# Performance work log

Measured on AMD Instinct MI355X. Metric: run time of the kernel, lower is better.

Reference implementation:

```python
import jax, jax.numpy as jnp
import numpy as np

N_T, N_C, N_M = 300000, 100000, 20000
D_IN, D, D_OUT = 390, 128, 64
H_PRE, H_POST = 256, 64


def _nrm(k, shape, scale=0.02):
    return jax.random.normal(k, shape, dtype=jnp.float32) * scale


def setup_inputs() -> dict:
    key = jax.random.key(0)
    ks = jax.random.split(key, 24)
    inp = {
        'input_features': jax.random.normal(ks[0], (N_T, D_IN), jnp.float32),
        'card_of_target': jax.random.randint(ks[1], (N_T,), 0, N_C, jnp.int32),
        'merchant_of_target': jax.random.randint(ks[2], (N_T,), 0, N_M, jnp.int32),
        # HeteroEmbedding tables for src types feeding 'target'
        'card_emb': _nrm(ks[3], (N_C, D)),
        'merch_emb': _nrm(ks[4], (N_M, D)),
        # target_preprocessing FFBlock (390 -> 256 -> 128, n_layers=2)
        'pre_Wi': _nrm(ks[5], (D_IN, H_PRE)), 'pre_bi': jnp.zeros((H_PRE,), jnp.float32),
        'pre_Wh': _nrm(ks[6], (H_PRE, H_PRE)), 'pre_bh': jnp.zeros((H_PRE,), jnp.float32),
        'pre_Wo': _nrm(ks[7], (H_PRE, D)), 'pre_bo': jnp.zeros((D,), jnp.float32),
        # conv1 / conv2: one GraphConv per etype; order:
        # 0=card->target, 1=merchant->target, 2=target->card, 3=target->merchant
        'conv1_W': _nrm(ks[8], (4, D, D)), 'conv1_b': jnp.zeros((4, D), jnp.float32),
        'conv2_W': _nrm(ks[9], (4, D, D)), 'conv2_b': jnp.zeros((4, D), jnp.float32),
        # conv3: dst=='target' -> D_OUT; dst!='target' -> 1
        'conv3_Wt': _nrm(ks[10], (2, D, D_OUT)), 'conv3_bt': jnp.zeros((2, D_OUT), jnp.float32),
        'conv3_Wo': _nrm(ks[11], (2, D, 1)), 'conv3_bo': jnp.zeros((2, 1), jnp.float32),
        # target_postprocessing FFBlock (64 -> 64 -> 1, n_layers=2)
        'post_Wi': _nrm(ks[12], (D_OUT, H_POST)), 'post_bi': jnp.zeros((H_POST,), jnp.float32),
        'post_Wh': _nrm(ks[13], (H_POST, H_POST)), 'post_bh': jnp.zeros((H_POST,), jnp.float32),
        'post_Wo': _nrm(ks[14], (H_POST, 1)), 'post_bo': jnp.zeros((1,), jnp.float32),
    }
    return inp


def _ff(x, Wi, bi, Wh, bh, Wo, bo, n_layers=2):
    h = jax.nn.relu(x @ Wi + bi)
    for _ in range(1, n_layers):
        h = jax.nn.relu(h @ Wh + bh)
    return h @ Wo + bo


def _deg(ids, n):
    # degree per node over edge endpoint list, clamped to >= 1 (DGL GraphConv)
    return jnp.maximum(jnp.zeros((n,), jnp.float32).at[ids].add(1.0), 1.0)


def _gconv(x_src, src, dst, n_dst, W, b, d_src, d_dst):
    # DGL GraphConv, norm='both': scale src by out_deg^-1/2, matmul,
    # sum messages onto dst, scale by in_deg^-1/2, add bias.
    h = (x_src * jax.lax.rsqrt(d_src)[:, None]) @ W          # [n_src, out]
    agg = jax.ops.segment_sum(h[src], dst, num_segments=n_dst)
    return agg * jax.lax.rsqrt(d_dst)[:, None] + b


def reference(input_features, card_of_target, merchant_of_target,
              card_emb, merch_emb,
              pre_Wi, pre_bi, pre_Wh, pre_bh, pre_Wo, pre_bo,
              conv1_W, conv1_b, conv2_W, conv2_b,
              conv3_Wt, conv3_bt, conv3_Wo, conv3_bo,
              post_Wi, post_bi, post_Wh, post_bh, post_Wo, post_bo):
    n_t, n_c, n_m = input_features.shape[0], card_emb.shape[0], merch_emb.shape[0]
    t_ids = jnp.arange(n_t, dtype=jnp.int32)
    d_c = _deg(card_of_target, n_c)      # card degree (in/out symmetric here)
    d_m = _deg(merchant_of_target, n_m)  # merchant degree
    d_t = _deg(t_ids, n_t)               # target degree (=1 per etype)

    tf = _ff(input_features, pre_Wi, pre_bi, pre_Wh, pre_bh, pre_Wo, pre_bo)

    # conv1 (HeteroGraphConv, aggregate='sum') + relu
    h1_t = (_gconv(card_emb, card_of_target, t_ids, n_t, conv1_W[0], conv1_b[0], d_c, d_t)
            + _gconv(merch_emb, merchant_of_target, t_ids, n_t, conv1_W[1], conv1_b[1], d_m, d_t))
    h1_c = _gconv(tf, t_ids, card_of_target, n_c, conv1_W[2], conv1_b[2], d_t, d_c)
    h1_m = _gconv(tf, t_ids, merchant_of_target, n_m, conv1_W[3], conv1_b[3], d_t, d_m)
    h1_t, h1_c, h1_m = jax.nn.relu(h1_t), jax.nn.relu(h1_c), jax.nn.relu(h1_m)

    # conv2 applied (conv_layers - 2) = 1 time
    h2_t, h2_c, h2_m = h1_t, h1_c, h1_m
    for _ in range(2, 3):
        n_t2 = (_gconv(h2_c, card_of_target, t_ids, n_t, conv2_W[0], conv2_b[0], d_c, d_t)
                + _gconv(h2_m, merchant_of_target, t_ids, n_t, conv2_W[1], conv2_b[1], d_m, d_t))
        n_c2 = _gconv(h2_t, t_ids, card_of_target, n_c, conv2_W[2], conv2_b[2], d_t, d_c)
        n_m2 = _gconv(h2_t, t_ids, merchant_of_target, n_m, conv2_W[3], conv2_b[3], d_t, d_m)
        h2_t, h2_c, h2_m = jax.nn.relu(n_t2), jax.nn.relu(n_c2), jax.nn.relu(n_m2)

    # conv3: D_OUT into target, 1 into non-target dsts; no relu
    h3_t = (_gconv(h2_c, card_of_target, t_ids, n_t, conv3_Wt[0], conv3_bt[0], d_c, d_t)
            + _gconv(h2_m, merchant_of_target, t_ids, n_t, conv3_Wt[1], conv3_bt[1], d_m, d_t))
    h3_c = _gconv(h2_t, t_ids, card_of_target, n_c, conv3_Wo[0], conv3_bo[0], d_t, d_c)
    h3_m = _gconv(h2_t, t_ids, merchant_of_target, n_m, conv3_Wo[1], conv3_bo[1], d_t, d_m)

    h3_t = _ff(h3_t, post_Wi, post_bi, post_Wh, post_bh, post_Wo, post_bo)
    return h3_t, h3_c, h3_m
```

## Files before the change

### kernel.cpp

```cpp
#include <hip/hip_runtime.h>


#define NT 300000
#define NC 100000
#define NM 20000
#define DIN 390
#define DD 128
#define DOUT 64
#define HPRE 256
#define HPOST 64

typedef _Float16 half8 __attribute__((ext_vector_type(8)));
typedef float f32x16 __attribute__((ext_vector_type(16)));
typedef float f32x4 __attribute__((ext_vector_type(4)));

#define LO_SCALE 512.0f
#define LO_INV   (1.0f / 512.0f)

__device__ __forceinline__ void split2(float x, _Float16& h, _Float16& l) {
    _Float16 hh = (_Float16)x;
    h = hh;
    l = (_Float16)((x - (float)hh) * LO_SCALE);
}

template<int TM, int TN, int WGM, int WGN>
__global__ __launch_bounds__(256, 3) void gemm_mfma(
    const float* __restrict__ A, const _Float16* __restrict__ Wh,
    const _Float16* __restrict__ Wl, const float* __restrict__ bias,
    const float* __restrict__ rowscale, float* __restrict__ C,
    int M, int K, int N, int Kpad, int relu)
{
    constexpr int BM = 32 * TM * WGM;
    constexpr int BN = 32 * TN * WGN;
    constexpr int RS = 40;
    __shared__ __align__(16) _Float16 Ah[BM * RS];
    __shared__ __align__(16) _Float16 Al[BM * RS];
    __shared__ __align__(16) _Float16 Bh[BN * RS];
    __shared__ __align__(16) _Float16 Bl[BN * RS];

    const int tid  = (int)threadIdx.x;
    const int lane = tid & 63;
    const int wave = tid >> 6;
    const int wm0 = (wave % WGM) * 32 * TM;
    const int wn0 = (wave / WGM) * 32 * TN;

    const int nbn = N / BN;
    const int tile = (int)blockIdx.x;
    const int bm = (tile / nbn) * BM;
    const int bn = (tile % nbn) * BN;

    f32x16 zz;
    #pragma unroll
    for (int i = 0; i < 16; ++i) zz[i] = 0.f;
    f32x16 acc_hh[TM][TN], acc_x[TM][TN];
    #pragma unroll
    for (int tm = 0; tm < TM; ++tm)
        #pragma unroll
        for (int tn = 0; tn < TN; ++tn) { acc_hh[tm][tn] = zz; acc_x[tm][tn] = zz; }

    constexpr int TPR  = 256 / BM;
    constexpr int KPT  = 32 / TPR;
    constexpr int FQ   = KPT / 4;
    const int sar = tid / TPR;
    const int sak = (tid % TPR) * KPT;
    const int agrow = bm + sar;
    const float* Aptr = A + (size_t)agrow * K;

    constexpr int TPRB = 256 / BN;
    constexpr int KPTB = 32 / TPRB;
    constexpr int NB   = KPTB / 8;
    const int sbr = tid / TPRB;
    const int sbk = (tid % TPRB) * KPTB;
    const _Float16* Bhp = Wh + (size_t)(bn + sbr) * Kpad + sbk;
    const _Float16* Blp = Wl + (size_t)(bn + sbr) * Kpad + sbk;

    const int ml  = lane & 31;
    const int klo = (lane >> 5) * 8;

    f32x4 areg[FQ];
    half8 bhreg[NB], blreg[NB];

    auto loadA = [&](int k0) {
        #pragma unroll
        for (int q = 0; q < FQ; ++q) {
            const int kb = k0 + sak + q * 4;
            f32x4 f = {0.f, 0.f, 0.f, 0.f};
            if (agrow < M) {
                if (kb + 3 < K) {
                    f = *(const f32x4*)(Aptr + kb);
                } else {
                    if (kb + 0 < K) f[0] = Aptr[kb + 0];
                    if (kb + 1 < K) f[1] = Aptr[kb + 1];
                    if (kb + 2 < K) f[2] = Aptr[kb + 2];
                    if (kb + 3 < K) f[3] = Aptr[kb + 3];
                }
            }
            areg[q] = f;
        }
    };
    auto loadB = [&](int k0) {
        #pragma unroll
        for (int j = 0; j < NB; ++j) {
            bhreg[j] = *(const half8*)(Bhp + k0 + j * 8);
            blreg[j] = *(const half8*)(Blp + k0 + j * 8);
        }
    };

    loadA(0);
    loadB(0);

    for (int k0 = 0; k0 < K; k0 += 32) {
        #pragma unroll
        for (int c = 0; c < FQ / 2; ++c) {
            half8 h, l;
            #pragma unroll
            for (int q = 0; q < 2; ++q) {
                #pragma unroll
                for (int j = 0; j < 4; ++j) {
                    _Float16 th, tl;
                    split2(areg[2 * c + q][j], th, tl);
                    h[q * 4 + j] = th;
                    l[q * 4 + j] = tl;
                }
            }
            *(half8*)&Ah[sar * RS + sak + c * 8] = h;
            *(half8*)&Al[sar * RS + sak + c * 8] = l;
        }
        #pragma unroll
        for (int j = 0; j < NB; ++j) {
            *(half8*)&Bh[sbr * RS + sbk + j * 8] = bhreg[j];
            *(half8*)&Bl[sbr * RS + sbk + j * 8] = blreg[j];
        }
        __syncthreads();

        if (k0 + 32 < K) { loadA(k0 + 32); loadB(k0 + 32); }

        #pragma unroll
        for (int ks = 0; ks < 2; ++ks) {
            const int kk = ks * 16 + klo;
            half8 fah[TM], fal[TM], fbh[TN], fbl[TN];
            #pragma unroll
            for (int t = 0; t < TM; ++t) {
                const int m = wm0 + t * 32 + ml;
                fah[t] = *(const half8*)&Ah[m * RS + kk];
                fal[t] = *(const half8*)&Al[m * RS + kk];
            }
            #pragma unroll
            for (int t = 0; t < TN; ++t) {
                const int n = wn0 + t * 32 + ml;
                fbh[t] = *(const half8*)&Bh[n * RS + kk];
                fbl[t] = *(const half8*)&Bl[n * RS + kk];
            }
            #pragma unroll
            for (int tm = 0; tm < TM; ++tm)
                #pragma unroll
                for (int tn = 0; tn < TN; ++tn) {
                    acc_hh[tm][tn] = __builtin_amdgcn_mfma_f32_32x32x16_f16(
                        fah[tm], fbh[tn], acc_hh[tm][tn], 0, 0, 0);
                    acc_x[tm][tn] = __builtin_amdgcn_mfma_f32_32x32x16_f16(
                        fah[tm], fbl[tn], acc_x[tm][tn], 0, 0, 0);
                    acc_x[tm][tn] = __builtin_amdgcn_mfma_f32_32x32x16_f16(
                        fal[tm], fbh[tn], acc_x[tm][tn], 0, 0, 0);
                }
        }
        __syncthreads();
    }

    const int r0 = 4 * (lane >> 5);
    #pragma unroll
    for (int tm = 0; tm < TM; ++tm) {
        #pragma unroll
        for (int tn = 0; tn < TN; ++tn) {
            const int gcol = bn + wn0 + tn * 32 + ml;
            const float bc = (bias != nullptr) ? bias[gcol] : 0.f;
            #pragma unroll
            for (int r = 0; r < 16; ++r) {
                const int grow = bm + wm0 + tm * 32 + (r & 3) + r0 + 8 * (r >> 2);
                if (grow < M) {
                    float v = acc_hh[tm][tn][r] + acc_x[tm][tn][r] * LO_INV;
                    if (rowscale != nullptr) v *= rowscale[grow];
                    v += bc;
                    if (relu) v = fmaxf(v, 0.f);
                    C[(size_t)grow * N + gcol] = v;
                }
            }
        }
    }
}

__global__ void split_w(const float* __restrict__ W, _Float16* __restrict__ hiT,
                        _Float16* __restrict__ loT, int K, int N, int Kpad, int nmat)
{
    int idx = blockIdx.x * blockDim.x + threadIdx.x;
    int total = nmat * N * Kpad;
    if (idx >= total) return;
    int e = idx / (N * Kpad);
    int rem = idx - e * (N * Kpad);
    int n = rem / Kpad;
    int k = rem - n * Kpad;
    float v = (k < K) ? W[((size_t)e * K + k) * N + n] : 0.f;
    _Float16 h = (_Float16)v;
    hiT[idx] = h;
    loT[idx] = (_Float16)((v - (float)h) * LO_SCALE);
}

__global__ void count_kernel(const int* __restrict__ card, const int* __restrict__ merch,
                             int* cnt_c, int* cnt_m, int n)
{
    int t = blockIdx.x * blockDim.x + threadIdx.x;
    if (t >= n) return;
    atomicAdd(&cnt_c[card[t]], 1);
    atomicAdd(&cnt_m[merch[t]], 1);
}

__global__ void rsqrt_kernel(const int* __restrict__ cnt, float* __restrict__ rs, int n)
{
    int i = blockIdx.x * blockDim.x + threadIdx.x;
    if (i >= n) return;
    int c = cnt[i];
    if (c < 1) c = 1;
    rs[i] = 1.0f / sqrtf((float)c);
}

__global__ __launch_bounds__(1024) void scan_excl(const int* __restrict__ cnt,
                                                  int* __restrict__ off, int n)
{
    __shared__ int wsum[16];
    const int tid = (int)threadIdx.x;
    const int lane = tid & 63, wid = tid >> 6;
    int carry = 0;
    for (int base = 0; base < n; base += 1024) {
        int i = base + tid;
        int v = (i < n) ? cnt[i] : 0;
        int x = v;
        #pragma unroll
        for (int d = 1; d < 64; d <<= 1) {
            int y = __shfl_up(x, d);
            if (lane >= d) x += y;
        }
        if (lane == 63) wsum[wid] = x;
        __syncthreads();
        int wpre = 0, tot = 0;
        #pragma unroll
        for (int w = 0; w < 16; ++w) {
            int s = wsum[w];
            if (w < wid) wpre += s;
            tot += s;
        }
        if (i < n) off[i] = carry + wpre + (x - v);
        carry += tot;
        __syncthreads();
    }
    if (tid == 0) off[n] = carry;
}

__global__ void fill_sorted(const int* __restrict__ ids, const int* __restrict__ off,
                            int* cur, int* __restrict__ srt, int n)
{
    int t = blockIdx.x * blockDim.x + threadIdx.x;
    if (t >= n) return;
    int c = ids[t];
    int p = atomicAdd(&cur[c], 1);
    srt[off[c] + p] = t;
}

__global__ void gather2_kernel(const float* __restrict__ hc, const float* __restrict__ hm,
                               const int* __restrict__ card, const int* __restrict__ merch,
                               const float* __restrict__ b0, const float* __restrict__ b1,
                               float* __restrict__ out, int n, int dim, int relu)
{
    int idx = blockIdx.x * blockDim.x + threadIdx.x;
    int per = dim >> 2;
    int t = idx / per;
    if (t >= n) return;
    int d4 = (idx % per) << 2;
    int c = card[t], m = merch[t];
    float4 a = *(const float4*)(hc + (size_t)c * dim + d4);
    float4 b = *(const float4*)(hm + (size_t)m * dim + d4);
    float4 v0 = *(const float4*)(b0 + d4);
    float4 v1 = *(const float4*)(b1 + d4);
    float4 r;
    r.x = a.x + b.x + v0.x + v1.x;
    r.y = a.y + b.y + v0.y + v1.y;
    r.z = a.z + b.z + v0.z + v1.z;
    r.w = a.w + b.w + v0.w + v1.w;
    if (relu) {
        r.x = fmaxf(r.x, 0.f); r.y = fmaxf(r.y, 0.f);
        r.z = fmaxf(r.z, 0.f); r.w = fmaxf(r.w, 0.f);
    }
    *(float4*)(out + (size_t)t * dim + d4) = r;
}

__global__ __launch_bounds__(256) void agg_csr_kernel(
    const float* __restrict__ proj, const int* __restrict__ off,
    const int* __restrict__ srt, const float* __restrict__ rs,
    const float* __restrict__ bias, float* __restrict__ out, int n, int relu)
{
    int node = blockIdx.x * 2 + ((int)threadIdx.x >> 7);
    int d = (int)threadIdx.x & 127;
    if (node >= n) return;
    int s = off[node], e = off[node + 1];
    float acc = 0.f;
    for (int i = s; i < e; ++i) {
        int t = srt[i];
        acc += proj[(size_t)t * 128 + d];
    }
    float v = acc * rs[node] + bias[d];
    if (relu) v = fmaxf(v, 0.f);
    out[(size_t)node * 128 + d] = v;
}

__global__ __launch_bounds__(256) void dot2_kernel(
    const float* __restrict__ h, const float* __restrict__ w0,
    const float* __restrict__ w1, float* __restrict__ s2, int n)
{
    int row = blockIdx.x * 4 + ((int)threadIdx.x >> 6);
    int l = (int)threadIdx.x & 63;
    if (row >= n) return;
    const float* x = h + (size_t)row * 128;
    float x0 = x[l], x1 = x[l + 64];
    float p0 = x0 * w0[l] + x1 * w0[l + 64];
    float p1 = x0 * w1[l] + x1 * w1[l + 64];
    #pragma unroll
    for (int o = 32; o > 0; o >>= 1) {
        p0 += __shfl_down(p0, o);
        p1 += __shfl_down(p1, o);
    }
    if (l == 0) { s2[(size_t)row * 2] = p0; s2[(size_t)row * 2 + 1] = p1; }
}

__global__ void agg_scalar_kernel(const float* __restrict__ s2, int which,
                                  const int* __restrict__ off, const int* __restrict__ srt,
                                  const float* __restrict__ rs, const float* __restrict__ bias,
                                  float* __restrict__ out, int n)
{
    int node = blockIdx.x * blockDim.x + threadIdx.x;
    if (node >= n) return;
    float acc = 0.f;
    int e = off[node + 1];
    for (int i = off[node]; i < e; ++i) acc += s2[(size_t)srt[i] * 2 + which];
    out[node] = acc * rs[node] + bias[0];
}

__global__ __launch_bounds__(256) void dot1_kernel(
    const float* __restrict__ h, const float* __restrict__ w,
    const float* __restrict__ b, float* __restrict__ out, int n)
{
    int row = blockIdx.x * 4 + ((int)threadIdx.x >> 6);
    int l = (int)threadIdx.x & 63;
    if (row >= n) return;
    float p = h[(size_t)row * 64 + l] * w[l];
    #pragma unroll
    for (int o = 32; o > 0; o >>= 1) p += __shfl_down(p, o);
    if (l == 0) out[row] = p + b[0];
}

static inline void gemmN(const float* A, const _Float16* wh, const _Float16* wl,
                         const float* bias, const float* rs, float* C,
                         int M, int K, int N, int Kpad, int relu, hipStream_t s)
{
    const int nbm = (M + 63) / 64;
    if (N % 128 == 0) {
        const int nbn = N / 128;
        gemm_mfma<1, 2, 2, 2><<<dim3(nbm * nbn), 256, 0, s>>>(
            A, wh, wl, bias, rs, C, M, K, N, Kpad, relu);
    } else {
        gemm_mfma<1, 1, 2, 2><<<dim3(nbm), 256, 0, s>>>(
            A, wh, wl, bias, rs, C, M, K, N, Kpad, relu);
    }
}

extern "C" void kernel_launch(void* const* d_in, const int* in_sizes, int n_in,
                              void* d_out, int out_size, void* d_ws, size_t ws_size,
                              hipStream_t stream)
{
    const float* x_in      = (const float*)d_in[0];
    const int*   card      = (const int*)d_in[1];
    const int*   merch     = (const int*)d_in[2];
    const float* card_emb  = (const float*)d_in[3];
    const float* merch_emb = (const float*)d_in[4];
    const float* pre_Wi = (const float*)d_in[5];
    const float* pre_bi = (const float*)d_in[6];
    const float* pre_Wh = (const float*)d_in[7];
    const float* pre_bh = (const float*)d_in[8];
    const float* pre_Wo = (const float*)d_in[9];
    const float* pre_bo = (const float*)d_in[10];
    const float* conv1_W = (const float*)d_in[11];
    const float* conv1_b = (const float*)d_in[12];
    const float* conv2_W = (const float*)d_in[13];
    const float* conv2_b = (const float*)d_in[14];
    const float* conv3_Wt = (const float*)d_in[15];
    const float* conv3_bt = (const float*)d_in[16];
    const float* conv3_Wo = (const float*)d_in[17];
    const float* conv3_bo = (const float*)d_in[18];
    const float* post_Wi = (const float*)d_in[19];
    const float* post_bi = (const float*)d_in[20];
    const float* post_Wh = (const float*)d_in[21];
    const float* post_bh = (const float*)d_in[22];
    const float* post_Wo = (const float*)d_in[23];
    const float* post_bo = (const float*)d_in[24];

    float* out = (float*)d_out;

    char* ws = (char*)d_ws;
    size_t off = 0;
    auto alloc = [&](size_t bytes) -> char* {
        char* p = ws + off;
        off += (bytes + 255) & ~(size_t)255;
        return p;
    };
    int* cnt_c = (int*)alloc((size_t)NC * 4);
    int* cnt_m = (int*)alloc((size_t)NM * 4);
    int* cur_c = (int*)alloc((size_t)NC * 4);
    int* cur_m = (int*)alloc((size_t)NM * 4);
    size_t zero_bytes = (size_t)((char*)(cur_m + NM) - (char*)cnt_c);
    int* off_c = (int*)alloc((size_t)(NC + 1) * 4);
    int* off_m = (int*)alloc((size_t)(NM + 1) * 4);
    int* srt_c = (int*)alloc((size_t)NT * 4);
    int* srt_m = (int*)alloc((size_t)NT * 4);
    float* rs_c = (float*)alloc((size_t)NC * 4);
    float* rs_m = (float*)alloc((size_t)NM * 4);

    const int KP_WI = 416;
    _Float16* wi_h  = (_Float16*)alloc((size_t)HPRE * KP_WI * 2);
    _Float16* wi_l  = (_Float16*)alloc((size_t)HPRE * KP_WI * 2);
    _Float16* wh_h  = (_Float16*)alloc((size_t)HPRE * HPRE * 2);
    _Float16* wh_l  = (_Float16*)alloc((size_t)HPRE * HPRE * 2);
    _Float16* wo_h  = (_Float16*)alloc((size_t)DD * HPRE * 2);
    _Float16* wo_l  = (_Float16*)alloc((size_t)DD * HPRE * 2);
    _Float16* c1_h  = (_Float16*)alloc((size_t)4 * DD * DD * 2);
    _Float16* c1_l  = (_Float16*)alloc((size_t)4 * DD * DD * 2);
    _Float16* c2_h  = (_Float16*)alloc((size_t)4 * DD * DD * 2);
    _Float16* c2_l  = (_Float16*)alloc((size_t)4 * DD * DD * 2);
    _Float16* c3_h  = (_Float16*)alloc((size_t)2 * DOUT * DD * 2);
    _Float16* c3_l  = (_Float16*)alloc((size_t)2 * DOUT * DD * 2);
    _Float16* pi_h  = (_Float16*)alloc((size_t)HPOST * DOUT * 2);
    _Float16* pi_l  = (_Float16*)alloc((size_t)HPOST * DOUT * 2);
    _Float16* ph_h  = (_Float16*)alloc((size_t)HPOST * HPOST * 2);
    _Float16* ph_l  = (_Float16*)alloc((size_t)HPOST * HPOST * 2);

    float* bufA = (float*)alloc((size_t)NT * HPRE * 4);
    float* bufB = (float*)alloc((size_t)NT * HPRE * 4);
    float* tf   = (float*)alloc((size_t)NT * DD * 4);
    float* proj = (float*)alloc((size_t)NT * DD * 4);
    float* h1_t = (float*)alloc((size_t)NT * DD * 4);
    float* h2_t = (float*)alloc((size_t)NT * DD * 4);
    float* h1_c = (float*)alloc((size_t)NC * DD * 4);
    float* h2_c = (float*)alloc((size_t)NC * DD * 4);
    float* hc_p = (float*)alloc((size_t)NC * DD * 4);
    float* h1_m = (float*)alloc((size_t)NM * DD * 4);
    float* h2_m = (float*)alloc((size_t)NM * DD * 4);
    float* hm_p = (float*)alloc((size_t)NM * DD * 4);
    float* s2   = (float*)alloc((size_t)NT * 2 * 4);
    float* h3t64 = h1_t;
    float* p1 = h2_t;
    float* p2 = h2_t + (size_t)NT * 64;
    (void)ws_size; (void)in_sizes; (void)n_in; (void)out_size;

    hipMemsetAsync(cnt_c, 0, zero_bytes, stream);
    count_kernel<<<(NT + 255) / 256, 256, 0, stream>>>(card, merch, cnt_c, cnt_m, NT);
    rsqrt_kernel<<<(NC + 255) / 256, 256, 0, stream>>>(cnt_c, rs_c, NC);
    rsqrt_kernel<<<(NM + 255) / 256, 256, 0, stream>>>(cnt_m, rs_m, NM);
    scan_excl<<<1, 1024, 0, stream>>>(cnt_c, off_c, NC);
    scan_excl<<<1, 1024, 0, stream>>>(cnt_m, off_m, NM);
    fill_sorted<<<(NT + 255) / 256, 256, 0, stream>>>(card, off_c, cur_c, srt_c, NT);
    fill_sorted<<<(NT + 255) / 256, 256, 0, stream>>>(merch, off_m, cur_m, srt_m, NT);

    auto splitw = [&](const float* W, _Float16* h, _Float16* l, int K, int N, int Kpad, int nmat) {
        int total = nmat * N * Kpad;
        split_w<<<(total + 255) / 256, 256, 0, stream>>>(W, h, l, K, N, Kpad, nmat);
    };
    splitw(pre_Wi,   wi_h, wi_l, DIN,  HPRE,  KP_WI, 1);
    splitw(pre_Wh,   wh_h, wh_l, HPRE, HPRE,  HPRE,  1);
    splitw(pre_Wo,   wo_h, wo_l, HPRE, DD,    HPRE,  1);
    splitw(conv1_W,  c1_h, c1_l, DD,   DD,    DD,    4);
    splitw(conv2_W,  c2_h, c2_l, DD,   DD,    DD,    4);
    splitw(conv3_Wt, c3_h, c3_l, DD,   DOUT,  DD,    2);
    splitw(post_Wi,  pi_h, pi_l, DOUT, HPOST, DOUT,  1);
    splitw(post_Wh,  ph_h, ph_l, HPOST,HPOST, HPOST, 1);

    const int WP = DD * DD;

    gemmN(x_in, wi_h, wi_l, pre_bi, nullptr, bufA, NT, DIN,  HPRE, KP_WI, 1, stream);
    gemmN(bufA, wh_h, wh_l, pre_bh, nullptr, bufB, NT, HPRE, HPRE, HPRE,  1, stream);
    gemmN(bufB, wo_h, wo_l, pre_bo, nullptr, tf,   NT, HPRE, DD,   HPRE,  0, stream);

    gemmN(card_emb,  c1_h + 0 * WP, c1_l + 0 * WP, nullptr, rs_c, hc_p, NC, DD, DD, DD, 0, stream);
    gemmN(merch_emb, c1_h + 1 * WP, c1_l + 1 * WP, nullptr, rs_m, hm_p, NM, DD, DD, DD, 0, stream);
    gather2_kernel<<<(NT * (DD / 4) + 255) / 256, 256, 0, stream>>>(
        hc_p, hm_p, card, merch, conv1_b, conv1_b + DD, h1_t, NT, DD, 1);
    gemmN(tf, c1_h + 2 * WP, c1_l + 2 * WP, nullptr, nullptr, proj, NT, DD, DD, DD, 0, stream);
    agg_csr_kernel<<<(NC + 1) / 2, 256, 0, stream>>>(proj, off_c, srt_c, rs_c,
                                                     conv1_b + 2 * DD, h1_c, NC, 1);
    gemmN(tf, c1_h + 3 * WP, c1_l + 3 * WP, nullptr, nullptr, proj, NT, DD, DD, DD, 0, stream);
    agg_csr_kernel<<<(NM + 1) / 2, 256, 0, stream>>>(proj, off_m, srt_m, rs_m,
                                                     conv1_b + 3 * DD, h1_m, NM, 1);

    gemmN(h1_c, c2_h + 0 * WP, c2_l + 0 * WP, nullptr, rs_c, hc_p, NC, DD, DD, DD, 0, stream);
    gemmN(h1_m, c2_h + 1 * WP, c2_l + 1 * WP, nullptr, rs_m, hm_p, NM, DD, DD, DD, 0, stream);
    gather2_kernel<<<(NT * (DD / 4) + 255) / 256, 256, 0, stream>>>(
        hc_p, hm_p, card, merch, conv2_b, conv2_b + DD, h2_t, NT, DD, 1);
    gemmN(h1_t, c2_h + 2 * WP, c2_l + 2 * WP, nullptr, nullptr, proj, NT, DD, DD, DD, 0, stream);
    agg_csr_kernel<<<(NC + 1) / 2, 256, 0, stream>>>(proj, off_c, srt_c, rs_c,
                                                     conv2_b + 2 * DD, h2_c, NC, 1);
    gemmN(h1_t, c2_h + 3 * WP, c2_l + 3 * WP, nullptr, nullptr, proj, NT, DD, DD, DD, 0, stream);
    agg_csr_kernel<<<(NM + 1) / 2, 256, 0, stream>>>(proj, off_m, srt_m, rs_m,
                                                     conv2_b + 3 * DD, h2_m, NM, 1);

    const int WP3 = DOUT * DD;
    gemmN(h2_c, c3_h + 0 * WP3, c3_l + 0 * WP3, nullptr, rs_c, hc_p, NC, DD, DOUT, DD, 0, stream);
    gemmN(h2_m, c3_h + 1 * WP3, c3_l + 1 * WP3, nullptr, rs_m, hm_p, NM, DD, DOUT, DD, 0, stream);
    gather2_kernel<<<(NT * (DOUT / 4) + 255) / 256, 256, 0, stream>>>(
        hc_p, hm_p, card, merch, conv3_bt, conv3_bt + DOUT, h3t64, NT, DOUT, 0);
    dot2_kernel<<<(NT + 3) / 4, 256, 0, stream>>>(h2_t, conv3_Wo, conv3_Wo + DD, s2, NT);
    agg_scalar_kernel<<<(NC + 255) / 256, 256, 0, stream>>>(s2, 0, off_c, srt_c, rs_c,
                                                            conv3_bo + 0, out + NT, NC);
    agg_scalar_kernel<<<(NM + 255) / 256, 256, 0, stream>>>(s2, 1, off_m, srt_m, rs_m,
                                                            conv3_bo + 1, out + NT + NC, NM);

    gemmN(h3t64, pi_h, pi_l, post_bi, nullptr, p1, NT, DOUT,  HPOST, DOUT,  1, stream);
    gemmN(p1,    ph_h, ph_l, post_bh, nullptr, p2, NT, HPOST, HPOST, HPOST, 1, stream);
    dot1_kernel<<<(NT + 3) / 4, 256, 0, stream>>>(p2, post_Wo, post_bo, out, NT);
}
```

Measured before the change: 2.791 ms.

## Store activations as pre-split fp16 hi/lo pairs and add direct-to-LDS GEMM

Producers (GEMM epilogues, gather, CSR aggregation) now write activations as fp16 hi/lo pairs instead of fp32. A new 512-thread GEMM loads these pre-split operands straight into LDS with global_load_lds, double-buffered and XOR-swizzled. This removes the per-tile fp32-to-fp16 split inside the GEMM and keeps total activation traffic the same (two fp16 halves equal one fp32), while the extra split kernels for the embedding tables add some one-off work. Buffers are padded to multiples of 128 rows so the loads need no bounds checks.

```diff
diff --git a/kernel.cpp b/kernel.cpp
--- a/kernel.cpp
+++ b/kernel.cpp
@@ -11,6 +11,7 @@
 #define HPOST 64
 
 typedef _Float16 half8 __attribute__((ext_vector_type(8)));
+typedef _Float16 half4v __attribute__((ext_vector_type(4)));
 typedef float f32x16 __attribute__((ext_vector_type(16)));
 typedef float f32x4 __attribute__((ext_vector_type(4)));
 
@@ -23,11 +24,147 @@
     l = (_Float16)((x - (float)hh) * LO_SCALE);
 }
 
+__device__ __forceinline__ void gload16(const _Float16* g, _Float16* l) {
+    __builtin_amdgcn_global_load_lds(
+        (const __attribute__((address_space(1))) void*)g,
+        (__attribute__((address_space(3))) void*)l, 16, 0, 0);
+}
+
+template<int TN>
+__global__ __launch_bounds__(512, 4) void gemm_ps(
+    const _Float16* __restrict__ Agh, const _Float16* __restrict__ Agl,
+    const _Float16* __restrict__ Bgh, const _Float16* __restrict__ Bgl,
+    const float* __restrict__ bias, const float* __restrict__ rowscale,
+    _Float16* __restrict__ Ch, _Float16* __restrict__ Cl,
+    float* __restrict__ C32,
+    int M, int Kpad, int N, int relu)
+{
+    constexpr int BM = 128;
+    constexpr int BN = 64 * TN;
+    constexpr int OFF_AH = 0;
+    constexpr int OFF_AL = 4096;
+    constexpr int OFF_BH = 8192;
+    constexpr int OFF_BL = 8192 + BN * 32;
+    constexpr int BUFH   = 8192 + 2 * BN * 32;
+    constexpr int NLD    = (TN == 2) ? 4 : 3;
+    __shared__ __align__(16) _Float16 smem[2 * BUFH];
+
+    const int tid  = (int)threadIdx.x;
+    const int lane = tid & 63;
+    const int wave = tid >> 6;
+    const int wm0  = (wave & 3) * 32;
+    const int wn0  = (wave >> 2) * 32 * TN;
+
+    const int nbn  = N / BN;
+    const int bm   = ((int)blockIdx.x / nbn) * BM;
+    const int bn   = ((int)blockIdx.x % nbn) * BN;
+
+    const int srow = lane >> 2;
+    const int xc8  = (((lane & 3) ^ (srow & 3)) << 3);
+    const size_t a_off = (size_t)(bm + wave * 16 + srow) * Kpad + xc8;
+    size_t b_off;
+    if constexpr (TN == 2) {
+        b_off = (size_t)(bn + wave * 16 + srow) * Kpad + xc8;
+    } else {
+        b_off = (size_t)(bn + (wave & 3) * 16 + srow) * Kpad + xc8;
+    }
+
+    auto stage = [&](int b, int k0) {
+        _Float16* sb = &smem[b * BUFH];
+        gload16(Agh + a_off + k0, sb + OFF_AH + wave * 512);
+        gload16(Agl + a_off + k0, sb + OFF_AL + wave * 512);
+        if constexpr (TN == 2) {
+            gload16(Bgh + b_off + k0, sb + OFF_BH + wave * 512);
+            gload16(Bgl + b_off + k0, sb + OFF_BL + wave * 512);
+        } else {
+            gload16((wave < 4 ? Bgh : Bgl) + b_off + k0,
+                    sb + (wave < 4 ? OFF_BH : OFF_BL) + (wave & 3) * 512);
+        }
+    };
+
+    f32x16 zz;
+    #pragma unroll
+    for (int i = 0; i < 16; ++i) zz[i] = 0.f;
+    f32x16 acc_hh[TN], acc_x[TN];
+    #pragma unroll
+    for (int t2 = 0; t2 < TN; ++t2) { acc_hh[t2] = zz; acc_x[t2] = zz; }
+
+    const int mlr = lane & 31;
+    const int hi5 = lane >> 5;
+    const int xr  = mlr & 3;
+
+    const int NS = Kpad >> 5;
+    stage(0, 0);
+
+    for (int t = 0; t < NS; ++t) {
+        if (t + 1 < NS) {
+            stage((t + 1) & 1, (t + 1) << 5);
+            asm volatile("s_waitcnt vmcnt(%0)" :: "n"(NLD) : "memory");
+        } else {
+            asm volatile("s_waitcnt vmcnt(0)" ::: "memory");
+        }
+        __builtin_amdgcn_s_barrier();
+        __builtin_amdgcn_sched_barrier(0);
+
+        const _Float16* sb = &smem[(t & 1) * BUFH];
+        #pragma unroll
+        for (int ks = 0; ks < 2; ++ks) {
+            const int xo = (((ks * 2 + hi5) ^ xr) << 3);
+            const half8 fah = *(const half8*)&sb[OFF_AH + (wm0 + mlr) * 32 + xo];
+            const half8 fal = *(const half8*)&sb[OFF_AL + (wm0 + mlr) * 32 + xo];
+            half8 fbh[TN], fbl[TN];
+            #pragma unroll
+            for (int t2 = 0; t2 < TN; ++t2) {
+                const int nn = wn0 + t2 * 32 + mlr;
+                fbh[t2] = *(const half8*)&sb[OFF_BH + nn * 32 + xo];
+                fbl[t2] = *(const half8*)&sb[OFF_BL + nn * 32 + xo];
+            }
+            #pragma unroll
+            for (int t2 = 0; t2 < TN; ++t2) {
+                acc_hh[t2] = __builtin_amdgcn_mfma_f32_32x32x16_f16(
+                    fah, fbh[t2], acc_hh[t2], 0, 0, 0);
+                acc_x[t2] = __builtin_amdgcn_mfma_f32_32x32x16_f16(
+                    fah, fbl[t2], acc_x[t2], 0, 0, 0);
+                acc_x[t2] = __builtin_amdgcn_mfma_f32_32x32x16_f16(
+                    fal, fbh[t2], acc_x[t2], 0, 0, 0);
+            }
+        }
+        __builtin_amdgcn_sched_barrier(0);
+        __builtin_amdgcn_s_barrier();
+    }
+
+    const int r0 = 4 * hi5;
+    #pragma unroll
+    for (int t2 = 0; t2 < TN; ++t2) {
+        const int gcol = bn + wn0 + t2 * 32 + mlr;
+        const float bc = (bias != nullptr) ? bias[gcol] : 0.f;
+        #pragma unroll
+        for (int r = 0; r < 16; ++r) {
+            const int grow = bm + wm0 + (r & 3) + r0 + 8 * (r >> 2);
+            if (grow < M) {
+                float v = acc_hh[t2][r] + acc_x[t2][r] * LO_INV;
+                if (rowscale != nullptr) v *= rowscale[grow];
+                v += bc;
+                if (relu) v = fmaxf(v, 0.f);
+                if (C32 != nullptr) {
+                    C32[(size_t)grow * N + gcol] = v;
+                } else {
+                    _Float16 hh, ll;
+                    split2(v, hh, ll);
+                    Ch[(size_t)grow * N + gcol] = hh;
+                    Cl[(size_t)grow * N + gcol] = ll;
+                }
+            }
+        }
+    }
+}
+
 template<int TM, int TN, int WGM, int WGN>
 __global__ __launch_bounds__(256, 3) void gemm_mfma(
     const float* __restrict__ A, const _Float16* __restrict__ Wh,
     const _Float16* __restrict__ Wl, const float* __restrict__ bias,
-    const float* __restrict__ rowscale, float* __restrict__ C,
+    const float* __restrict__ rowscale,
+    float* __restrict__ C32, _Float16* __restrict__ Ch, _Float16* __restrict__ Cl,
     int M, int K, int N, int Kpad, int relu)
 {
     constexpr int BM = 32 * TM * WGM;
@@ -181,7 +318,14 @@
                     if (rowscale != nullptr) v *= rowscale[grow];
                     v += bc;
                     if (relu) v = fmaxf(v, 0.f);
-                    C[(size_t)grow * N + gcol] = v;
+                    if (C32 != nullptr) {
+                        C32[(size_t)grow * N + gcol] = v;
+                    } else {
+                        _Float16 hh, ll;
+                        split2(v, hh, ll);
+                        Ch[(size_t)grow * N + gcol] = hh;
+                        Cl[(size_t)grow * N + gcol] = ll;
+                    }
                 }
             }
         }
@@ -204,6 +348,31 @@
     loT[idx] = (_Float16)((v - (float)h) * LO_SCALE);
 }
 
+__global__ void split_a(const float* __restrict__ X, _Float16* __restrict__ xh,
+                        _Float16* __restrict__ xl, int M, int Mpad, int K)
+{
+    int idx = blockIdx.x * blockDim.x + threadIdx.x;
+    int per = K >> 3;
+    int total = Mpad * per;
+    if (idx >= total) return;
+    int row = idx / per;
+    int k = (idx - row * per) << 3;
+    half8 h, l;
+    if (row < M) {
+        #pragma unroll
+        for (int j = 0; j < 8; ++j) {
+            _Float16 th, tl;
+            split2(X[(size_t)row * K + k + j], th, tl);
+            h[j] = th; l[j] = tl;
+        }
+    } else {
+        #pragma unroll
+        for (int j = 0; j < 8; ++j) { h[j] = (_Float16)0.f; l[j] = (_Float16)0.f; }
+    }
+    *(half8*)&xh[(size_t)row * K + k] = h;
+    *(half8*)&xl[(size_t)row * K + k] = l;
+}
+
 __global__ void count_kernel(const int* __restrict__ card, const int* __restrict__ merch,
                              int* cnt_c, int* cnt_m, int n)
 {
@@ -267,7 +436,8 @@
 __global__ void gather2_kernel(const float* __restrict__ hc, const float* __restrict__ hm,
                                const int* __restrict__ card, const int* __restrict__ merch,
                                const float* __restrict__ b0, const float* __restrict__ b1,
-                               float* __restrict__ out, int n, int dim, int relu)
+                               float* __restrict__ out32, _Float16* __restrict__ oh,
+                               _Float16* __restrict__ ol, int n, int dim, int relu)
 {
     int idx = blockIdx.x * blockDim.x + threadIdx.x;
     int per = dim >> 2;
@@ -288,13 +458,25 @@
         r.x = fmaxf(r.x, 0.f); r.y = fmaxf(r.y, 0.f);
         r.z = fmaxf(r.z, 0.f); r.w = fmaxf(r.w, 0.f);
     }
-    *(float4*)(out + (size_t)t * dim + d4) = r;
+    if (out32 != nullptr) {
+        *(float4*)(out32 + (size_t)t * dim + d4) = r;
+    } else {
+        half4v h, l;
+        _Float16 th, tl;
+        split2(r.x, th, tl); h[0] = th; l[0] = tl;
+        split2(r.y, th, tl); h[1] = th; l[1] = tl;
+        split2(r.z, th, tl); h[2] = th; l[2] = tl;
+        split2(r.w, th, tl); h[3] = th; l[3] = tl;
+        *(half4v*)&oh[(size_t)t * dim + d4] = h;
+        *(half4v*)&ol[(size_t)t * dim + d4] = l;
+    }
 }
 
 __global__ __launch_bounds__(256) void agg_csr_kernel(
     const float* __restrict__ proj, const int* __restrict__ off,
     const int* __restrict__ srt, const float* __restrict__ rs,
-    const float* __restrict__ bias, float* __restrict__ out, int n, int relu)
+    const float* __restrict__ bias, _Float16* __restrict__ oh,
+    _Float16* __restrict__ ol, int n, int relu)
 {
     int node = blockIdx.x * 2 + ((int)threadIdx.x >> 7);
     int d = (int)threadIdx.x & 127;
@@ -307,7 +489,10 @@
     }
     float v = acc * rs[node] + bias[d];
     if (relu) v = fmaxf(v, 0.f);
-    out[(size_t)node * 128 + d] = v;
+    _Float16 hh, ll;
+    split2(v, hh, ll);
+    oh[(size_t)node * 128 + d] = hh;
+    ol[(size_t)node * 128 + d] = ll;
 }
 
 __global__ __launch_bounds__(256) void dot2_kernel(
@@ -355,20 +540,22 @@
     if (l == 0) out[row] = p + b[0];
 }
 
-static inline void gemmN(const float* A, const _Float16* wh, const _Float16* wl,
-                         const float* bias, const float* rs, float* C,
-                         int M, int K, int N, int Kpad, int relu, hipStream_t s)
-{
-    const int nbm = (M + 63) / 64;
+static inline void gemm_ps_launch(const _Float16* Ah, const _Float16* Al,
+    const _Float16* Bh, const _Float16* Bl, const float* bias, const float* rs,
+    _Float16* Ch, _Float16* Cl, float* C32,
+    int M, int Kpad, int N, int relu, hipStream_t s)
+{
+    const int nbm = (M + 127) / 128;
     if (N % 128 == 0) {
-        const int nbn = N / 128;
-        gemm_mfma<1, 2, 2, 2><<<dim3(nbm * nbn), 256, 0, s>>>(
-            A, wh, wl, bias, rs, C, M, K, N, Kpad, relu);
+        gemm_ps<2><<<dim3(nbm * (N / 128)), 512, 0, s>>>(
+            Ah, Al, Bh, Bl, bias, rs, Ch, Cl, C32, M, Kpad, N, relu);
     } else {
-        gemm_mfma<1, 1, 2, 2><<<dim3(nbm), 256, 0, s>>>(
-            A, wh, wl, bias, rs, C, M, K, N, Kpad, relu);
-    }
-}
+        gemm_ps<1><<<dim3(nbm), 512, 0, s>>>(
+            Ah, Al, Bh, Bl, bias, rs, Ch, Cl, C32, M, Kpad, N, relu);
+    }
+}
+
+#define PAD128(x) ((((x) + 127) / 128) * 128)
 
 extern "C" void kernel_launch(void* const* d_in, const int* in_sizes, int n_in,
                               void* d_out, int out_size, void* d_ws, size_t ws_size,
@@ -402,6 +589,10 @@
 
     float* out = (float*)d_out;
 
+    const int MTP = PAD128(NT);
+    const int MCP = PAD128(NC);
+    const int MMP = PAD128(NM);
+
     char* ws = (char*)d_ws;
     size_t off = 0;
     auto alloc = [&](size_t bytes) -> char* {
@@ -439,22 +630,37 @@
     _Float16* ph_h  = (_Float16*)alloc((size_t)HPOST * HPOST * 2);
     _Float16* ph_l  = (_Float16*)alloc((size_t)HPOST * HPOST * 2);
 
-    float* bufA = (float*)alloc((size_t)NT * HPRE * 4);
-    float* bufB = (float*)alloc((size_t)NT * HPRE * 4);
-    float* tf   = (float*)alloc((size_t)NT * DD * 4);
-    float* proj = (float*)alloc((size_t)NT * DD * 4);
-    float* h1_t = (float*)alloc((size_t)NT * DD * 4);
-    float* h2_t = (float*)alloc((size_t)NT * DD * 4);
-    float* h1_c = (float*)alloc((size_t)NC * DD * 4);
-    float* h2_c = (float*)alloc((size_t)NC * DD * 4);
-    float* hc_p = (float*)alloc((size_t)NC * DD * 4);
-    float* h1_m = (float*)alloc((size_t)NM * DD * 4);
-    float* h2_m = (float*)alloc((size_t)NM * DD * 4);
-    float* hm_p = (float*)alloc((size_t)NM * DD * 4);
+    _Float16* ce_h   = (_Float16*)alloc((size_t)MCP * DD * 2);
+    _Float16* ce_l   = (_Float16*)alloc((size_t)MCP * DD * 2);
+    _Float16* me_h   = (_Float16*)alloc((size_t)MMP * DD * 2);
+    _Float16* me_l   = (_Float16*)alloc((size_t)MMP * DD * 2);
+    _Float16* bufA_h = (_Float16*)alloc((size_t)MTP * HPRE * 2);
+    _Float16* bufA_l = (_Float16*)alloc((size_t)MTP * HPRE * 2);
+    _Float16* bufB_h = (_Float16*)alloc((size_t)MTP * HPRE * 2);
+    _Float16* bufB_l = (_Float16*)alloc((size_t)MTP * HPRE * 2);
+    _Float16* tf_h   = (_Float16*)alloc((size_t)MTP * DD * 2);
+    _Float16* tf_l   = (_Float16*)alloc((size_t)MTP * DD * 2);
+    _Float16* h1t_h  = (_Float16*)alloc((size_t)MTP * DD * 2);
+    _Float16* h1t_l  = (_Float16*)alloc((size_t)MTP * DD * 2);
+    _Float16* h1c_h  = (_Float16*)alloc((size_t)MCP * DD * 2);
+    _Float16* h1c_l  = (_Float16*)alloc((size_t)MCP * DD * 2);
+    _Float16* h1m_h  = (_Float16*)alloc((size_t)MMP * DD * 2);
+    _Float16* h1m_l  = (_Float16*)alloc((size_t)MMP * DD * 2);
+    _Float16* h2c_h  = (_Float16*)alloc((size_t)MCP * DD * 2);
+    _Float16* h2c_l  = (_Float16*)alloc((size_t)MCP * DD * 2);
+    _Float16* h2m_h  = (_Float16*)alloc((size_t)MMP * DD * 2);
+    _Float16* h2m_l  = (_Float16*)alloc((size_t)MMP * DD * 2);
+    _Float16* h3_h   = (_Float16*)alloc((size_t)MTP * DOUT * 2);
+    _Float16* h3_l   = (_Float16*)alloc((size_t)MTP * DOUT * 2);
+    _Float16* p1_h   = (_Float16*)alloc((size_t)MTP * DOUT * 2);
+    _Float16* p1_l   = (_Float16*)alloc((size_t)MTP * DOUT * 2);
+
+    float* proj = (float*)alloc((size_t)MTP * DD * 4);
+    float* h2_t = (float*)alloc((size_t)MTP * DD * 4);
+    float* hc_p = (float*)alloc((size_t)MCP * DD * 4);
+    float* hm_p = (float*)alloc((size_t)MMP * DD * 4);
+    float* p2   = (float*)alloc((size_t)MTP * DOUT * 4);
     float* s2   = (float*)alloc((size_t)NT * 2 * 4);
-    float* h3t64 = h1_t;
-    float* p1 = h2_t;
-    float* p2 = h2_t + (size_t)NT * 64;
     (void)ws_size; (void)in_sizes; (void)n_in; (void)out_size;
 
     hipMemsetAsync(cnt_c, 0, zero_bytes, stream);
@@ -479,46 +685,71 @@
     splitw(post_Wi,  pi_h, pi_l, DOUT, HPOST, DOUT,  1);
     splitw(post_Wh,  ph_h, ph_l, HPOST,HPOST, HPOST, 1);
 
-    const int WP = DD * DD;
-
-    gemmN(x_in, wi_h, wi_l, pre_bi, nullptr, bufA, NT, DIN,  HPRE, KP_WI, 1, stream);
-    gemmN(bufA, wh_h, wh_l, pre_bh, nullptr, bufB, NT, HPRE, HPRE, HPRE,  1, stream);
-    gemmN(bufB, wo_h, wo_l, pre_bo, nullptr, tf,   NT, HPRE, DD,   HPRE,  0, stream);
-
-    gemmN(card_emb,  c1_h + 0 * WP, c1_l + 0 * WP, nullptr, rs_c, hc_p, NC, DD, DD, DD, 0, stream);
-    gemmN(merch_emb, c1_h + 1 * WP, c1_l + 1 * WP, nullptr, rs_m, hm_p, NM, DD, DD, DD, 0, stream);
+    split_a<<<((MCP * (DD / 8)) + 255) / 256, 256, 0, stream>>>(card_emb, ce_h, ce_l, NC, MCP, DD);
+    split_a<<<((MMP * (DD / 8)) + 255) / 256, 256, 0, stream>>>(merch_emb, me_h, me_l, NM, MMP, DD);
+
+    const int WP  = DD * DD;
+    const int WP3 = DOUT * DD;
+
+    {
+        const int nbm = (NT + 63) / 64;
+        gemm_mfma<1, 2, 2, 2><<<dim3(nbm * 2), 256, 0, stream>>>(
+            x_in, wi_h, wi_l, pre_bi, nullptr, nullptr, bufA_h, bufA_l,
+            NT, DIN, HPRE, KP_WI, 1);
+    }
+    gemm_ps_launch(bufA_h, bufA_l, wh_h, wh_l, pre_bh, nullptr,
+                   bufB_h, bufB_l, nullptr, NT, HPRE, HPRE, 1, stream);
+    gemm_ps_launch(bufB_h, bufB_l, wo_h, wo_l, pre_bo, nullptr,
+                   tf_h, tf_l, nullptr, NT, HPRE, DD, 0, stream);
+
+    gemm_ps_launch(ce_h, ce_l, c1_h + 0 * WP, c1_l + 0 * WP, nullptr, rs_c,
+                   nullptr, nullptr, hc_p, NC, DD, DD, 0, stream);
+    gemm_ps_launch(me_h, me_l, c1_h + 1 * WP, c1_l + 1 * WP, nullptr, rs_m,
+                   nullptr, nullptr, hm_p, NM, DD, DD, 0, stream);
     gather2_kernel<<<(NT * (DD / 4) + 255) / 256, 256, 0, stream>>>(
-        hc_p, hm_p, card, merch, conv1_b, conv1_b + DD, h1_t, NT, DD, 1);
-    gemmN(tf, c1_h + 2 * WP, c1_l + 2 * WP, nullptr, nullptr, proj, NT, DD, DD, DD, 0, stream);
+        hc_p, hm_p, card, merch, conv1_b, conv1_b + DD,
+        nullptr, h1t_h, h1t_l, NT, DD, 1);
+    gemm_ps_launch(tf_h, tf_l, c1_h + 2 * WP, c1_l + 2 * WP, nullptr, nullptr,
+                   nullptr, nullptr, proj, NT, DD, DD, 0, stream);
     agg_csr_kernel<<<(NC + 1) / 2, 256, 0, stream>>>(proj, off_c, srt_c, rs_c,
-                                                     conv1_b + 2 * DD, h1_c, NC, 1);
-    gemmN(tf, c1_h + 3 * WP, c1_l + 3 * WP, nullptr, nullptr, proj, NT, DD, DD, DD, 0, stream);
+                                                     conv1_b + 2 * DD, h1c_h, h1c_l, NC, 1);
+    gemm_ps_launch(tf_h, tf_l, c1_h + 3 * WP, c1_l + 3 * WP, nullptr, nullptr,
+                   nullptr, nullptr, proj, NT, DD, DD, 0, stream);
     agg_csr_kernel<<<(NM + 1) / 2, 256, 0, stream>>>(proj, off_m, srt_m, rs_m,
-                                                     conv1_b + 3 * DD, h1_m, NM, 1);
-
-    gemmN(h1_c, c2_h + 0 * WP, c2_l + 0 * WP, nullptr, rs_c, hc_p, NC, DD, DD, DD, 0, stream);
-    gemmN(h1_m, c2_h + 1 * WP, c2_l + 1 * WP, nullptr, rs_m, hm_p, NM, DD, DD, DD, 0, stream);
+                                                     conv1_b + 3 * DD, h1m_h, h1m_l, NM, 1);
+
+    gemm_ps_launch(h1c_h, h1c_l, c2_h + 0 * WP, c2_l + 0 * WP, nullptr, rs_c,
+                   nullptr, nullptr, hc_p, NC, DD, DD, 0, stream);
+    gemm_ps_launch(h1m_h, h1m_l, c2_h + 1 * WP, c2_l + 1 * WP, nullptr, rs_m,
+                   nullptr, nullptr, hm_p, NM, DD, DD, 0, stream);
     gather2_kernel<<<(NT * (DD / 4) + 255) / 256, 256, 0, stream>>>(
-        hc_p, hm_p, card, merch, conv2_b, conv2_b + DD, h2_t, NT, DD, 1);
-    gemmN(h1_t, c2_h + 2 * WP, c2_l + 2 * WP, nullptr, nullptr, proj, NT, DD, DD, DD, 0, stream);
+        hc_p, hm_p, card, merch, conv2_b, conv2_b + DD,
+        h2_t, nullptr, nullptr, NT, DD, 1);
+    gemm_ps_launch(h1t_h, h1t_l, c2_h + 2 * WP, c2_l + 2 * WP, nullptr, nullptr,
+                   nullptr, nullptr, proj, NT, DD, DD, 0, stream);
     agg_csr_kernel<<<(NC + 1) / 2, 256, 0, stream>>>(proj, off_c, srt_c, rs_c,
-                                                     conv2_b + 2 * DD, h2_c, NC, 1);
-    gemmN(h1_t, c2_h + 3 * WP, c2_l + 3 * WP, nullptr, nullptr, proj, NT, DD, DD, DD, 0, stream);
+                                                     conv2_b + 2 * DD, h2c_h, h2c_l, NC, 1);
+    gemm_ps_launch(h1t_h, h1t_l, c2_h + 3 * WP, c2_l + 3 * WP, nullptr, nullptr,
+                   nullptr, nullptr, proj, NT, DD, DD, 0, stream);
     agg_csr_kernel<<<(NM + 1) / 2, 256, 0, stream>>>(proj, off_m, srt_m, rs_m,
-                                                     conv2_b + 3 * DD, h2_m, NM, 1);
-
-    const int WP3 = DOUT * DD;
-    gemmN(h2_c, c3_h + 0 * WP3, c3_l + 0 * WP3, nullptr, rs_c, hc_p, NC, DD, DOUT, DD, 0, stream);
-    gemmN(h2_m, c3_h + 1 * WP3, c3_l + 1 * WP3, nullptr, rs_m, hm_p, NM, DD, DOUT, DD, 0, stream);
+                                                     conv2_b + 3 * DD, h2m_h, h2m_l, NM, 1);
+
+    gemm_ps_launch(h2c_h, h2c_l, c3_h + 0 * WP3, c3_l + 0 * WP3, nullptr, rs_c,
+                   nullptr, nullptr, hc_p, NC, DD, DOUT, 0, stream);
+    gemm_ps_launch(h2m_h, h2m_l, c3_h + 1 * WP3, c3_l + 1 * WP3, nullptr, rs_m,
+                   nullptr, nullptr, hm_p, NM, DD, DOUT, 0, stream);
     gather2_kernel<<<(NT * (DOUT / 4) + 255) / 256, 256, 0, stream>>>(
-        hc_p, hm_p, card, merch, conv3_bt, conv3_bt + DOUT, h3t64, NT, DOUT, 0);
+        hc_p, hm_p, card, merch, conv3_bt, conv3_bt + DOUT,
+        nullptr, h3_h, h3_l, NT, DOUT, 0);
     dot2_kernel<<<(NT + 3) / 4, 256, 0, stream>>>(h2_t, conv3_Wo, conv3_Wo + DD, s2, NT);
     agg_scalar_kernel<<<(NC + 255) / 256, 256, 0, stream>>>(s2, 0, off_c, srt_c, rs_c,
                                                             conv3_bo + 0, out + NT, NC);
     agg_scalar_kernel<<<(NM + 255) / 256, 256, 0, stream>>>(s2, 1, off_m, srt_m, rs_m,
                                                             conv3_bo + 1, out + NT + NC, NM);
 
-    gemmN(h3t64, pi_h, pi_l, post_bi, nullptr, p1, NT, DOUT,  HPOST, DOUT,  1, stream);
-    gemmN(p1,    ph_h, ph_l, post_bh, nullptr, p2, NT, HPOST, HPOST, HPOST, 1, stream);
+    gemm_ps_launch(h3_h, h3_l, pi_h, pi_l, post_bi, nullptr,
+                   p1_h, p1_l, nullptr, NT, DOUT, HPOST, 1, stream);
+    gemm_ps_launch(p1_h, p1_l, ph_h, ph_l, post_bh, nullptr,
+                   nullptr, nullptr, p2, NT, HPOST, HPOST, 1, stream);
     dot1_kernel<<<(NT + 3) / 4, 256, 0, stream>>>(p2, post_Wo, post_bo, out, NT);
 }
```

Measured after the change: 2.761 ms. Within noise of the previous version (-1.1%).
